# Kernel optimization log

Measured on AMD Instinct MI355X. Metric: run time of the kernel, lower is better.

Reference implementation:

```python
import jax, jax.numpy as jnp
import numpy as np

B, S = 64, 512
DC, DB = 200, 200            # embed_char_dim, embed_bichar_dim
HID = 300                    # linear out / lstm input
H = 300                      # rnn_hidden_dim
VC, VB = 10000, 200000       # char / bichar vocab
INPUT_DIM = (DC + DB) * 2    # 800


def lstm_scan(x_seq, W_hh):
    # x_seq: [S, B, 4H] = x @ W_ih.T + b_ih + b_hh, precomputed for all steps
    Bq = x_seq.shape[1]
    h0 = jnp.zeros((Bq, H), x_seq.dtype)
    c0 = jnp.zeros((Bq, H), x_seq.dtype)

    def step(carry, x_t):
        h, c = carry
        gates = x_t + h @ W_hh.T                 # [B, 4H]
        i, f, g, o = jnp.split(gates, 4, axis=-1)
        i = jax.nn.sigmoid(i)
        f = jax.nn.sigmoid(f)
        g = jnp.tanh(g)
        o = jax.nn.sigmoid(o)
        c = f * c + i * g
        h = o * jnp.tanh(c)
        return (h, c), h

    _, hs = jax.lax.scan(step, (h0, c0), x_seq)
    return hs                                    # [S, B, H]


def setup_inputs() -> dict:
    key = jax.random.key(0)
    ks = jax.random.split(key, 20)
    inp = {
        'char_features': jax.random.randint(ks[0], (B, S), 0, VC),
        'bichar_left_features': jax.random.randint(ks[1], (B, S), 0, VB),
        'bichar_right_features': jax.random.randint(ks[2], (B, S), 0, VB),
        'static_char_features': jax.random.randint(ks[3], (B, S), 0, VC),
        'static_bichar_left_features': jax.random.randint(ks[4], (B, S), 0, VB),
        'static_bichar_right_features': jax.random.randint(ks[5], (B, S), 0, VB),
        # embedding tables (padding-id row zeroing omitted; random rows)
        'char_embed': jax.random.normal(ks[6], (VC, DC), jnp.float32) * 0.1,
        'bichar_embed': jax.random.normal(ks[7], (VB, DB), jnp.float32) * 0.1,
        'static_char_embed': jax.random.uniform(ks[8], (VC, DC), jnp.float32, -0.12, 0.12),
        'static_bichar_embed': jax.random.uniform(ks[9], (VB, DB), jnp.float32, -0.12, 0.12),
        # linear: [HID, INPUT_DIM]
        'W_lin': jax.random.normal(ks[10], (HID, INPUT_DIM), jnp.float32) * (1.0 / np.sqrt(INPUT_DIM)),
        'b_lin': jax.random.normal(ks[11], (HID,), jnp.float32) * 0.01,
        # LSTM cells (b = b_ih + b_hh folded)
        'Wih_l': jax.random.normal(ks[12], (4 * H, HID), jnp.float32) * (1.0 / np.sqrt(HID)),
        'Whh_l': jax.random.normal(ks[13], (4 * H, H), jnp.float32) * (1.0 / np.sqrt(H)),
        'b_l': jax.random.normal(ks[14], (4 * H,), jnp.float32) * 0.01,
        'Wih_r': jax.random.normal(ks[15], (4 * H, HID), jnp.float32) * (1.0 / np.sqrt(HID)),
        'Whh_r': jax.random.normal(ks[16], (4 * H, H), jnp.float32) * (1.0 / np.sqrt(H)),
        'b_r': jax.random.normal(ks[17], (4 * H,), jnp.float32) * 0.01,
    }
    return inp


def reference(char_features, bichar_left_features, bichar_right_features,
              static_char_features, static_bichar_left_features, static_bichar_right_features,
              char_embed, bichar_embed, static_char_embed, static_bichar_embed,
              W_lin, b_lin, Wih_l, Whh_l, b_l, Wih_r, Whh_r, b_r):
    # embedding lookups (dropout is identity in eval mode)
    cf = char_embed[char_features]                       # [B,S,DC]
    scf = static_char_embed[static_char_features]        # [B,S,DC]
    bl = bichar_embed[bichar_left_features]              # [B,S,DB]
    br = bichar_embed[bichar_right_features]             # [B,S,DB]
    sbl = static_bichar_embed[static_bichar_left_features]
    sbr = static_bichar_embed[static_bichar_right_features]

    left = jnp.concatenate([cf, scf, bl, sbl], axis=-1)   # [B,S,INPUT_DIM]
    right = jnp.concatenate([cf, scf, br, sbr], axis=-1)
    left = jnp.tanh(left @ W_lin.T + b_lin)               # [B,S,HID]
    right = jnp.tanh(right @ W_lin.T + b_lin)

    # precompute input contributions for all timesteps, then scan the recurrence
    xl = jnp.einsum('bsd,gd->sbg', left, Wih_l) + b_l     # [S,B,4H]
    hs_l = lstm_scan(xl, Whh_l)                            # [S,B,H]

    xr = jnp.einsum('bsd,gd->sbg', right, Wih_r) + b_r
    hs_r = lstm_scan(xr[::-1], Whh_r)[::-1]               # right-to-left LSTM

    out = jnp.concatenate([hs_l.transpose(1, 0, 2), hs_r.transpose(1, 0, 2)], axis=-1)
    return out                                             # [B,S,2H]
```

## Files before the change

kernel.cpp:

```cpp
#include <hip/hip_runtime.h>
#include <hip/hip_bf16.h>

#define S_LEN 512
#define BATCH 64
#define DC    200
#define HID   300
#define H4    1200
#define IN_DIM 800
#define G_SPLIT 10

typedef __attribute__((ext_vector_type(8))) short short8b;
typedef __attribute__((ext_vector_type(4))) float f32x4;
typedef __attribute__((ext_vector_type(4))) int   i32x4;

__device__ __forceinline__ float sigmoidf_(float x) { return 1.0f / (1.0f + __expf(-x)); }
__device__ __forceinline__ float tanhf_(float x)    { return 2.0f / (1.0f + __expf(-2.0f * x)) - 1.0f; }

__global__ void k_prep_w(const float* __restrict__ Whh_l, const float* __restrict__ Whh_r,
                         const float* __restrict__ Wih_l, const float* __restrict__ Wih_r,
                         __hip_bfloat16* __restrict__ Whh_p, __hip_bfloat16* __restrict__ Wih_p) {
    int i = blockIdx.x * 256 + threadIdx.x;
    if (i >= 2 * 1280 * 320) return;
    int slot = i % 320;
    int R = (i / 320) % 1280;
    int d = i / (320 * 1280);
    int g = R >> 7, local = R & 127;
    float vh = 0.f, vi = 0.f;
    if (local < 120) {
        int q = local / 30, jj = local % 30;
        int n = q * 300 + g * 30 + jj;
        const float* Whh = d ? Whh_r : Whh_l;
        const float* Wih = d ? Wih_r : Wih_l;
        int g2 = slot >> 5, jj2 = slot & 31;
        if (jj2 < 30) vh = Whh[n * 300 + g2 * 30 + jj2];
        if (slot < 300) vi = Wih[n * 300 + slot];
    }
    Whh_p[i] = __float2bfloat16(vh);
    Wih_p[i] = __float2bfloat16(vi);
}

__global__ void k_prep_misc(const float* __restrict__ b_l, const float* __restrict__ b_r,
                            int* __restrict__ hb_st,
                            float* __restrict__ bias_p) {
    int i = blockIdx.x * 256 + threadIdx.x;
    if (i < 102400) hb_st[i] = 0;
    if (i < 2 * 1280) {
        int d = i / 1280, R = i % 1280;
        int g = R >> 7, local = R & 127;
        float v = 0.f;
        if (local < 120) { int q = local / 30, jj = local % 30; v = (d ? b_r : b_l)[q * 300 + g * 30 + jj]; }
        bias_p[i] = v;
    }
}

__global__ __launch_bounds__(256) void k_lin(
    const int* __restrict__ cf, const int* __restrict__ bl, const int* __restrict__ br,
    const int* __restrict__ scf, const int* __restrict__ sbl, const int* __restrict__ sbr,
    const float* __restrict__ ce, const float* __restrict__ be,
    const float* __restrict__ sce, const float* __restrict__ sbe,
    const float* __restrict__ W, const float* __restrict__ bias,
    __hip_bfloat16* __restrict__ outL, __hip_bfloat16* __restrict__ outR)
{
    const int z = blockIdx.y;
    const int* dynIdx  = z ? br  : bl;
    const int* statIdx = z ? sbr : sbl;
    __hip_bfloat16* outp = z ? outR : outL;
    const int m0 = blockIdx.x * 64;

    __shared__ __align__(16) __hip_bfloat16 sA[64][40];
    __shared__ __align__(16) __hip_bfloat16 sB[320][40];
    const int t = threadIdx.x, lane = t & 63, wv = t >> 6;

    const int rA = t >> 2, c8A = (t & 3) * 8;
    const int mA = m0 + rA;
    const int idc = cf[mA], idsc = scf[mA], idd = dynIdx[mA], ids = statIdx[mA];

    f32x4 acc[4][5] = {};

    for (int k0 = 0; k0 < IN_DIM; k0 += 32) {
        {
            int k = k0 + c8A;
            int seg = k / 200, kin = k - seg * 200;
            const float* tab = (seg == 0) ? ce : (seg == 1) ? sce : (seg == 2) ? be : sbe;
            int id = (seg == 0) ? idc : (seg == 1) ? idsc : (seg == 2) ? idd : ids;
            const float* tp = tab + (size_t)id * DC + kin;
            f32x4 v0 = *reinterpret_cast<const f32x4*>(tp);
            f32x4 v1 = *reinterpret_cast<const f32x4*>(tp + 4);
            union { short8b v; __hip_bfloat16 h[8]; } u;
#pragma unroll
            for (int q = 0; q < 4; ++q) { u.h[q] = __float2bfloat16(v0[q]); u.h[4 + q] = __float2bfloat16(v1[q]); }
            *reinterpret_cast<short8b*>(&sA[rA][c8A]) = u.v;
        }
#pragma unroll
        for (int j = 0; j < 5; ++j) {
            int i = t + j * 256;
            int n = i >> 2, ch = (i & 3) * 8;
            f32x4 v0 = {0, 0, 0, 0}, v1 = {0, 0, 0, 0};
            if (n < HID) {
                const float* wp = W + (size_t)n * IN_DIM + k0 + ch;
                v0 = *reinterpret_cast<const f32x4*>(wp);
                v1 = *reinterpret_cast<const f32x4*>(wp + 4);
            }
            union { short8b v; __hip_bfloat16 h[8]; } u;
#pragma unroll
            for (int q = 0; q < 4; ++q) { u.h[q] = __float2bfloat16(v0[q]); u.h[4 + q] = __float2bfloat16(v1[q]); }
            *reinterpret_cast<short8b*>(&sB[n][ch]) = u.v;
        }
        __syncthreads();
        const int kl = (lane >> 4) * 8, bb = lane & 15;
#pragma unroll
        for (int mt = 0; mt < 4; ++mt) {
            short8b af = *reinterpret_cast<const short8b*>(&sA[mt * 16 + bb][kl]);
#pragma unroll
            for (int nt = 0; nt < 5; ++nt) {
                short8b bf = *reinterpret_cast<const short8b*>(&sB[(wv * 5 + nt) * 16 + bb][kl]);
                acc[mt][nt] = __builtin_amdgcn_mfma_f32_16x16x32_bf16(af, bf, acc[mt][nt], 0, 0, 0);
            }
        }
        __syncthreads();
    }
    const int bb = lane & 15;
#pragma unroll
    for (int mt = 0; mt < 4; ++mt)
#pragma unroll
        for (int nt = 0; nt < 5; ++nt) {
            int p = (wv * 5 + nt) * 16 + bb;
            float bv = (p < HID) ? bias[p] : 0.f;
#pragma unroll
            for (int r = 0; r < 4; ++r) {
                int m = m0 + mt * 16 + (lane >> 4) * 4 + r;
                float val = (p < HID) ? tanhf_(acc[mt][nt][r] + bv) : 0.f;
                outp[(size_t)m * 320 + p] = __float2bfloat16(val);
            }
        }
}

__global__ __launch_bounds__(256) void k_xgemm(
    const __hip_bfloat16* __restrict__ A,
    const __hip_bfloat16* __restrict__ Wih_p,
    const float* __restrict__ bias_p,
    __hip_bfloat16* __restrict__ Xout)
{
    const int dir = blockIdx.z;
    const int m0 = blockIdx.x * 64;
    const int n0 = blockIdx.y * 128;
    const __hip_bfloat16* Ad = A + (size_t)dir * 32768 * 320;
    const __hip_bfloat16* Wd = Wih_p + (size_t)dir * 1280 * 320;
    const float* bd = bias_p + dir * 1280;
    __hip_bfloat16* Xd = Xout + (size_t)dir * 512 * 64 * 1280;

    __shared__ __align__(16) __hip_bfloat16 sA[64][40];
    __shared__ __align__(16) __hip_bfloat16 sB[128][40];
    const int t = threadIdx.x, lane = t & 63, wv = t >> 6;
    f32x4 acc[4][2] = {};

    for (int k0 = 0; k0 < 320; k0 += 32) {
        {
            int r = t >> 2, kg = (t & 3) * 8;
            *reinterpret_cast<short8b*>(&sA[r][kg]) =
                *reinterpret_cast<const short8b*>(Ad + (size_t)(m0 + r) * 320 + k0 + kg);
        }
#pragma unroll
        for (int i = 0; i < 2; ++i) {
            int c = t + i * 256;
            int r = c >> 2, kg = (c & 3) * 8;
            *reinterpret_cast<short8b*>(&sB[r][kg]) =
                *reinterpret_cast<const short8b*>(Wd + (size_t)(n0 + r) * 320 + k0 + kg);
        }
        __syncthreads();
        const int kl = (lane >> 4) * 8;
#pragma unroll
        for (int mt = 0; mt < 4; ++mt) {
            short8b af = *reinterpret_cast<const short8b*>(&sA[mt * 16 + (lane & 15)][kl]);
#pragma unroll
            for (int nt = 0; nt < 2; ++nt) {
                short8b bf = *reinterpret_cast<const short8b*>(&sB[(wv * 2 + nt) * 16 + (lane & 15)][kl]);
                acc[mt][nt] = __builtin_amdgcn_mfma_f32_16x16x32_bf16(af, bf, acc[mt][nt], 0, 0, 0);
            }
        }
        __syncthreads();
    }
#pragma unroll
    for (int mt = 0; mt < 4; ++mt)
#pragma unroll
        for (int nt = 0; nt < 2; ++nt) {
            int p = n0 + (wv * 2 + nt) * 16 + (lane & 15);
            float bv = bd[p];
#pragma unroll
            for (int r = 0; r < 4; ++r) {
                int m = m0 + mt * 16 + (lane >> 4) * 4 + r;
                int b = m >> 9, s = m & 511;
                Xd[(size_t)(s * 64 + b) * 1280 + p] = __float2bfloat16(acc[mt][nt][r] + bv);
            }
        }
}

__global__ __launch_bounds__(256) void k_rec(
    const __hip_bfloat16* __restrict__ X,
    const __hip_bfloat16* __restrict__ Whh_p,
    i32x4* __restrict__ hb_st,
    float* __restrict__ out)
{
    const int bid = blockIdx.x;
    const int dir = bid / (4 * G_SPLIT);
    const int grp = (bid / G_SPLIT) % 4;
    const int g   = bid % G_SPLIT;
    const int t = threadIdx.x;
    const int lane = t & 63, wv = t >> 6;
    const int b0 = grp * 16;

    __shared__ __align__(16) __hip_bfloat16 sHi[16][328];
    __shared__ __align__(16) __hip_bfloat16 sLo[16][328];
    __shared__ float sG[16][132];
    unsigned* sHiW = (unsigned*)sHi;
    unsigned* sLoW = (unsigned*)sLo;

    const int n0 = wv * 32;
    const int bb = lane & 15;
    const int hi4 = lane >> 4;

    short8b wB0[10], wB1[10];
    {
        const __hip_bfloat16* Wsrc = Whh_p + ((size_t)dir * 1280 + g * 128) * 320;
#pragma unroll
        for (int kt = 0; kt < 10; ++kt) {
            wB0[kt] = *reinterpret_cast<const short8b*>(Wsrc + (size_t)(n0 + bb) * 320 + kt * 32 + hi4 * 8);
            wB1[kt] = *reinterpret_cast<const short8b*>(Wsrc + (size_t)(n0 + 16 + bb) * 320 + kt * 32 + hi4 * 8);
        }
    }
    for (int i = t; i < 16 * 164; i += 256) { sHiW[i] = 0; sLoW[i] = 0; }
    __syncthreads();

    float cst[6] = {};

    __hip_bfloat16 xa[8];
    {
        const int s0 = dir ? (S_LEN - 1) : 0;
        const __hip_bfloat16* xp = X + (((size_t)dir * 512 + s0) * 64 + b0) * 1280 + g * 128;
#pragma unroll
        for (int r = 0; r < 4; ++r) {
            int m = hi4 * 4 + r;
            xa[r]     = xp[(size_t)m * 1280 + n0 + bb];
            xa[4 + r] = xp[(size_t)m * 1280 + n0 + 16 + bb];
        }
    }

    for (int tau = 0; tau < S_LEN; ++tau) {
        const int s = dir ? (S_LEN - 1 - tau) : tau;
        const int par = tau & 1;

        i32x4 ch[7];
        const i32x4* hbase = hb_st + ((size_t)(dir * 2 + par) * 64 + b0) * 100;
        for (;;) {
            bool ok = true;
#pragma unroll
            for (int k = 0; k < 7; ++k) {
                int idx = t + k * 256;
                if (idx < 1600)
                    asm volatile("global_load_dwordx4 %0, %1, off sc0 sc1"
                                 : "=v"(ch[k]) : "v"(hbase + idx) : "memory");
            }
            asm volatile("s_waitcnt vmcnt(0)" ::: "memory");
#pragma unroll
            for (int k = 0; k < 7; ++k) {
                int idx = t + k * 256;
                if (idx < 1600 && ch[k][0] != tau) ok = false;
            }
            if (ok) break;
            __builtin_amdgcn_s_sleep(1);
        }
        __builtin_amdgcn_sched_barrier(0);

#pragma unroll
        for (int k = 0; k < 7; ++k) {
            int idx = t + k * 256;
            if (idx < 1600) {
                int b = idx / 100, rem = idx - b * 100;
                int g2 = rem / 10, c = rem - g2 * 10;
                int chi = (c < 5) ? c : c - 5;
                unsigned* dst = ((c < 5) ? sHiW : sLoW) + b * 164 + g2 * 16 + chi * 3;
                dst[0] = (unsigned)ch[k][1];
                dst[1] = (unsigned)ch[k][2];
                dst[2] = (unsigned)ch[k][3];
            }
        }
        __syncthreads();

        f32x4 acc0, acc1;
#pragma unroll
        for (int r = 0; r < 4; ++r) {
            acc0[r] = __bfloat162float(xa[r]);
            acc1[r] = __bfloat162float(xa[4 + r]);
        }
#pragma unroll
        for (int kt = 0; kt < 10; ++kt) {
            short8b ahi = *reinterpret_cast<const short8b*>(&sHi[bb][kt * 32 + hi4 * 8]);
            short8b alo = *reinterpret_cast<const short8b*>(&sLo[bb][kt * 32 + hi4 * 8]);
            acc0 = __builtin_amdgcn_mfma_f32_16x16x32_bf16(ahi, wB0[kt], acc0, 0, 0, 0);
            acc1 = __builtin_amdgcn_mfma_f32_16x16x32_bf16(ahi, wB1[kt], acc1, 0, 0, 0);
            acc0 = __builtin_amdgcn_mfma_f32_16x16x32_bf16(alo, wB0[kt], acc0, 0, 0, 0);
            acc1 = __builtin_amdgcn_mfma_f32_16x16x32_bf16(alo, wB1[kt], acc1, 0, 0, 0);
        }
#pragma unroll
        for (int r = 0; r < 4; ++r) {
            int m = hi4 * 4 + r;
            sG[m][n0 + bb] = acc0[r];
            sG[m][n0 + 16 + bb] = acc1[r];
        }
        __syncthreads();

        if (t < 80) {
            int b = t / 5, c5 = t - (b * 5), jj0 = c5 * 6;
            float hv[6];
            unsigned hius[6], lous[6];
#pragma unroll
            for (int u = 0; u < 6; ++u) {
                int jj = jj0 + u;
                float ig = sigmoidf_(sG[b][jj]);
                float fg = sigmoidf_(sG[b][30 + jj]);
                float gg = tanhf_(sG[b][60 + jj]);
                float og = sigmoidf_(sG[b][90 + jj]);
                float cn = fg * cst[u] + ig * gg;
                cst[u] = cn;
                float h = og * tanhf_(cn);
                hv[u] = h;
                __hip_bfloat16 hb_ = __float2bfloat16(h);
                float lof = h - __bfloat162float(hb_);
                __hip_bfloat16 lb_ = __float2bfloat16(lof);
                union { __hip_bfloat16 x; unsigned short u16; } ch1{hb_}, ch2{lb_};
                hius[u] = ch1.u16;
                lous[u] = ch2.u16;
            }
            i32x4 dhi, dlo;
            dhi[0] = tau + 1; dhi[1] = (int)(hius[0] | (hius[1] << 16));
            dhi[2] = (int)(hius[2] | (hius[3] << 16)); dhi[3] = (int)(hius[4] | (hius[5] << 16));
            dlo[0] = tau + 1; dlo[1] = (int)(lous[0] | (lous[1] << 16));
            dlo[2] = (int)(lous[2] | (lous[3] << 16)); dlo[3] = (int)(lous[4] | (lous[5] << 16));
            i32x4* pb = hb_st + ((size_t)(dir * 2 + (par ^ 1)) * 64 + b0 + b) * 100 + g * 10 + c5;
            asm volatile("s_waitcnt vmcnt(0)" ::: "memory");
            asm volatile("global_store_dwordx4 %0, %1, off sc0 sc1" :: "v"(pb), "v"(dhi) : "memory");
            asm volatile("global_store_dwordx4 %0, %1, off sc0 sc1" :: "v"(pb + 5), "v"(dlo) : "memory");
            float* op = out + ((size_t)(b0 + b) * S_LEN + s) * 600 + dir * 300 + g * 30 + jj0;
#pragma unroll
            for (int u = 0; u < 6; ++u) op[u] = hv[u];
        }

        if (tau < S_LEN - 1) {
            const int sn = dir ? (s - 1) : (s + 1);
            const __hip_bfloat16* xp = X + (((size_t)dir * 512 + sn) * 64 + b0) * 1280 + g * 128;
#pragma unroll
            for (int r = 0; r < 4; ++r) {
                int m = hi4 * 4 + r;
                xa[r]     = xp[(size_t)m * 1280 + n0 + bb];
                xa[4 + r] = xp[(size_t)m * 1280 + n0 + 16 + bb];
            }
        }
    }
}

extern "C" void kernel_launch(void* const* d_in, const int* in_sizes, int n_in,
                              void* d_out, int out_size, void* d_ws, size_t ws_size,
                              hipStream_t stream) {
    const int*   cf    = (const int*)d_in[0];
    const int*   bl    = (const int*)d_in[1];
    const int*   br    = (const int*)d_in[2];
    const int*   scf   = (const int*)d_in[3];
    const int*   sbl   = (const int*)d_in[4];
    const int*   sbr   = (const int*)d_in[5];
    const float* ce    = (const float*)d_in[6];
    const float* be    = (const float*)d_in[7];
    const float* sce   = (const float*)d_in[8];
    const float* sbe   = (const float*)d_in[9];
    const float* Wlin  = (const float*)d_in[10];
    const float* blin  = (const float*)d_in[11];
    const float* Wih_l = (const float*)d_in[12];
    const float* Whh_l = (const float*)d_in[13];
    const float* b_l   = (const float*)d_in[14];
    const float* Wih_r = (const float*)d_in[15];
    const float* Whh_r = (const float*)d_in[16];
    const float* b_r   = (const float*)d_in[17];
    float* out = (float*)d_out;

    char* ws = (char*)d_ws;
    __hip_bfloat16* A_b    = (__hip_bfloat16*)(ws);
    __hip_bfloat16* A_l    = A_b;
    __hip_bfloat16* A_r    = A_b + (size_t)32768 * 320;
    __hip_bfloat16* X      = (__hip_bfloat16*)(ws + 41943040);
    __hip_bfloat16* Whh_p  = (__hip_bfloat16*)(ws + 209715200);
    __hip_bfloat16* Wih_p  = (__hip_bfloat16*)(ws + 211353600);
    float*          bias_p = (float*)(ws + 212992000);
    i32x4*          hb_st  = (i32x4*)(ws + 213002240);

    k_prep_w<<<dim3((2 * 1280 * 320 + 255) / 256), dim3(256), 0, stream>>>(
        Whh_l, Whh_r, Wih_l, Wih_r, Whh_p, Wih_p);
    k_prep_misc<<<dim3(1280), dim3(256), 0, stream>>>(b_l, b_r, (int*)hb_st, bias_p);
    k_lin<<<dim3(512, 2), dim3(256), 0, stream>>>(cf, bl, br, scf, sbl, sbr,
                                                  ce, be, sce, sbe, Wlin, blin,
                                                  A_l, A_r);
    k_xgemm<<<dim3(512, 10, 2), dim3(256), 0, stream>>>(A_b, Wih_p, bias_p, X);
    k_rec<<<dim3(80), dim3(256), 0, stream>>>(X, Whh_p, hb_st, out);
}
```

Before: 2.288 ms.

## Exchange hidden state via 8-byte atomics with packed step stamp

The cross-block hidden-state exchange in the recurrent kernel is rebuilt. Each 16-byte record that carried 6 values plus a separate stamp becomes an 8-byte record of 3 bf16 values with the stamp packed in the top half. Stores now use atomic swap and polling uses atomic OR with zero, and polling only retries chunks not yet seen. The gate-update stage is also split across 160 threads instead of 80. The aim is lower store-to-load visibility latency and less redundant polling traffic per step. The cost is roughly twice as many, smaller atomic operations per step, and the stamp is limited to 16 bits.

Result: slower. 2.981 ms (+30.3%).

```diff
diff --git a/kernel.cpp b/kernel.cpp
--- a/kernel.cpp
+++ b/kernel.cpp
@@ -11,7 +11,7 @@
 
 typedef __attribute__((ext_vector_type(8))) short short8b;
 typedef __attribute__((ext_vector_type(4))) float f32x4;
-typedef __attribute__((ext_vector_type(4))) int   i32x4;
+typedef __attribute__((ext_vector_type(2))) int   i32x2;
 
 __device__ __forceinline__ float sigmoidf_(float x) { return 1.0f / (1.0f + __expf(-x)); }
 __device__ __forceinline__ float tanhf_(float x)    { return 2.0f / (1.0f + __expf(-2.0f * x)) - 1.0f; }
@@ -40,10 +40,10 @@
 }
 
 __global__ void k_prep_misc(const float* __restrict__ b_l, const float* __restrict__ b_r,
-                            int* __restrict__ hb_st,
+                            int* __restrict__ hb,
                             float* __restrict__ bias_p) {
     int i = blockIdx.x * 256 + threadIdx.x;
-    if (i < 102400) hb_st[i] = 0;
+    if (i < 102400) hb[i] = 0;
     if (i < 2 * 1280) {
         int d = i / 1280, R = i % 1280;
         int g = R >> 7, local = R & 127;
@@ -198,7 +198,7 @@
 __global__ __launch_bounds__(256) void k_rec(
     const __hip_bfloat16* __restrict__ X,
     const __hip_bfloat16* __restrict__ Whh_p,
-    i32x4* __restrict__ hb_st,
+    i32x2* __restrict__ hb,
     float* __restrict__ out)
 {
     const int bid = blockIdx.x;
@@ -212,6 +212,8 @@
     __shared__ __align__(16) __hip_bfloat16 sHi[16][328];
     __shared__ __align__(16) __hip_bfloat16 sLo[16][328];
     __shared__ float sG[16][132];
+    unsigned short* sHiU = (unsigned short*)sHi;
+    unsigned short* sLoU = (unsigned short*)sLo;
     unsigned* sHiW = (unsigned*)sHi;
     unsigned* sLoW = (unsigned*)sLo;
 
@@ -231,7 +233,7 @@
     for (int i = t; i < 16 * 164; i += 256) { sHiW[i] = 0; sLoW[i] = 0; }
     __syncthreads();
 
-    float cst[6] = {};
+    float cst[3] = {};
 
     __hip_bfloat16 xa[8];
     {
@@ -245,43 +247,50 @@
         }
     }
 
+    const i32x2 zero2 = {0, 0};
+
     for (int tau = 0; tau < S_LEN; ++tau) {
         const int s = dir ? (S_LEN - 1 - tau) : tau;
         const int par = tau & 1;
 
-        i32x4 ch[7];
-        const i32x4* hbase = hb_st + ((size_t)(dir * 2 + par) * 64 + b0) * 100;
+        i32x2 q[13];
+        unsigned done = 0;
+        const i32x2* hbase = hb + ((size_t)(dir * 2 + par) * 64 + b0) * 200;
         for (;;) {
-            bool ok = true;
-#pragma unroll
-            for (int k = 0; k < 7; ++k) {
+#pragma unroll
+            for (int k = 0; k < 13; ++k) {
                 int idx = t + k * 256;
-                if (idx < 1600)
-                    asm volatile("global_load_dwordx4 %0, %1, off sc0 sc1"
-                                 : "=v"(ch[k]) : "v"(hbase + idx) : "memory");
+                if (idx < 3200 && !((done >> k) & 1))
+                    asm volatile("global_atomic_or_x2 %0, %1, %2, off sc0 sc1"
+                                 : "=v"(q[k]) : "v"(hbase + idx), "v"(zero2) : "memory");
             }
             asm volatile("s_waitcnt vmcnt(0)" ::: "memory");
-#pragma unroll
-            for (int k = 0; k < 7; ++k) {
+            bool all = true;
+#pragma unroll
+            for (int k = 0; k < 13; ++k) {
                 int idx = t + k * 256;
-                if (idx < 1600 && ch[k][0] != tau) ok = false;
-            }
-            if (ok) break;
+                if (idx < 3200 && !((done >> k) & 1)) {
+                    if ((((unsigned)q[k][1]) >> 16) == (unsigned)tau) done |= 1u << k;
+                    else all = false;
+                }
+            }
+            if (all) break;
             __builtin_amdgcn_s_sleep(1);
         }
         __builtin_amdgcn_sched_barrier(0);
 
 #pragma unroll
-        for (int k = 0; k < 7; ++k) {
+        for (int k = 0; k < 13; ++k) {
             int idx = t + k * 256;
-            if (idx < 1600) {
-                int b = idx / 100, rem = idx - b * 100;
-                int g2 = rem / 10, c = rem - g2 * 10;
-                int chi = (c < 5) ? c : c - 5;
-                unsigned* dst = ((c < 5) ? sHiW : sLoW) + b * 164 + g2 * 16 + chi * 3;
-                dst[0] = (unsigned)ch[k][1];
-                dst[1] = (unsigned)ch[k][2];
-                dst[2] = (unsigned)ch[k][3];
+            if (idx < 3200) {
+                int b = idx / 200, r = idx - b * 200;
+                int buf = r / 100, j = r - buf * 100;
+                int jt = j / 10;
+                int slot = jt * 32 + (j - jt * 10) * 3;
+                unsigned short* dst = (buf ? sLoU : sHiU) + b * 328 + slot;
+                dst[0] = (unsigned short)(q[k][0] & 0xffff);
+                dst[1] = (unsigned short)(((unsigned)q[k][0]) >> 16);
+                dst[2] = (unsigned short)(q[k][1] & 0xffff);
             }
         }
         __syncthreads();
@@ -309,13 +318,13 @@
         }
         __syncthreads();
 
-        if (t < 80) {
-            int b = t / 5, c5 = t - (b * 5), jj0 = c5 * 6;
-            float hv[6];
-            unsigned hius[6], lous[6];
-#pragma unroll
-            for (int u = 0; u < 6; ++u) {
-                int jj = jj0 + u;
+        if (t < 160) {
+            int b = t / 10, jq = t - b * 10;
+            float hv3[3];
+            unsigned hu[3], lu[3];
+#pragma unroll
+            for (int u = 0; u < 3; ++u) {
+                int jj = 3 * jq + u;
                 float ig = sigmoidf_(sG[b][jj]);
                 float fg = sigmoidf_(sG[b][30 + jj]);
                 float gg = tanhf_(sG[b][60 + jj]);
@@ -323,26 +332,25 @@
                 float cn = fg * cst[u] + ig * gg;
                 cst[u] = cn;
                 float h = og * tanhf_(cn);
-                hv[u] = h;
+                hv3[u] = h;
                 __hip_bfloat16 hb_ = __float2bfloat16(h);
                 float lof = h - __bfloat162float(hb_);
                 __hip_bfloat16 lb_ = __float2bfloat16(lof);
-                union { __hip_bfloat16 x; unsigned short u16; } ch1{hb_}, ch2{lb_};
-                hius[u] = ch1.u16;
-                lous[u] = ch2.u16;
-            }
-            i32x4 dhi, dlo;
-            dhi[0] = tau + 1; dhi[1] = (int)(hius[0] | (hius[1] << 16));
-            dhi[2] = (int)(hius[2] | (hius[3] << 16)); dhi[3] = (int)(hius[4] | (hius[5] << 16));
-            dlo[0] = tau + 1; dlo[1] = (int)(lous[0] | (lous[1] << 16));
-            dlo[2] = (int)(lous[2] | (lous[3] << 16)); dlo[3] = (int)(lous[4] | (lous[5] << 16));
-            i32x4* pb = hb_st + ((size_t)(dir * 2 + (par ^ 1)) * 64 + b0 + b) * 100 + g * 10 + c5;
-            asm volatile("s_waitcnt vmcnt(0)" ::: "memory");
-            asm volatile("global_store_dwordx4 %0, %1, off sc0 sc1" :: "v"(pb), "v"(dhi) : "memory");
-            asm volatile("global_store_dwordx4 %0, %1, off sc0 sc1" :: "v"(pb + 5), "v"(dlo) : "memory");
-            float* op = out + ((size_t)(b0 + b) * S_LEN + s) * 600 + dir * 300 + g * 30 + jj0;
-#pragma unroll
-            for (int u = 0; u < 6; ++u) op[u] = hv[u];
+                union { __hip_bfloat16 x; unsigned short u16; } c1{hb_}, c2{lb_};
+                hu[u] = c1.u16;
+                lu[u] = c2.u16;
+            }
+            unsigned stamp = (unsigned)(tau + 1);
+            i32x2 dhi, dlo;
+            dhi[0] = (int)(hu[0] | (hu[1] << 16));
+            dhi[1] = (int)(hu[2] | (stamp << 16));
+            dlo[0] = (int)(lu[0] | (lu[1] << 16));
+            dlo[1] = (int)(lu[2] | (stamp << 16));
+            i32x2* pb = hb + ((size_t)(dir * 2 + (par ^ 1)) * 64 + b0 + b) * 200 + g * 10 + jq;
+            asm volatile("global_atomic_swap_x2 %0, %1, off sc1" :: "v"(pb), "v"(dhi) : "memory");
+            asm volatile("global_atomic_swap_x2 %0, %1, off sc1" :: "v"(pb + 100), "v"(dlo) : "memory");
+            float* op = out + ((size_t)(b0 + b) * S_LEN + s) * 600 + dir * 300 + g * 30 + 3 * jq;
+            op[0] = hv3[0]; op[1] = hv3[1]; op[2] = hv3[2];
         }
 
         if (tau < S_LEN - 1) {
@@ -389,14 +397,14 @@
     __hip_bfloat16* Whh_p  = (__hip_bfloat16*)(ws + 209715200);
     __hip_bfloat16* Wih_p  = (__hip_bfloat16*)(ws + 211353600);
     float*          bias_p = (float*)(ws + 212992000);
-    i32x4*          hb_st  = (i32x4*)(ws + 213002240);
+    i32x2*          hb     = (i32x2*)(ws + 213002240);
 
     k_prep_w<<<dim3((2 * 1280 * 320 + 255) / 256), dim3(256), 0, stream>>>(
         Whh_l, Whh_r, Wih_l, Wih_r, Whh_p, Wih_p);
-    k_prep_misc<<<dim3(1280), dim3(256), 0, stream>>>(b_l, b_r, (int*)hb_st, bias_p);
+    k_prep_misc<<<dim3(1280), dim3(256), 0, stream>>>(b_l, b_r, (int*)hb, bias_p);
     k_lin<<<dim3(512, 2), dim3(256), 0, stream>>>(cf, bl, br, scf, sbl, sbr,
                                                   ce, be, sce, sbe, Wlin, blin,
                                                   A_l, A_r);
     k_xgemm<<<dim3(512, 10, 2), dim3(256), 0, stream>>>(A_b, Wih_p, bias_p, X);
-    k_rec<<<dim3(80), dim3(256), 0, stream>>>(X, Whh_p, hb_st, out);
-}
+    k_rec<<<dim3(80), dim3(256), 0, stream>>>(X, Whh_p, hb, out);
+}
```

## Store recurrent state chunks with flags in place and poll only missing chunks

Applied to the files above, without the earlier changes.

The recurrent hidden-state exchange now copies each 16-byte chunk, including its step flag, directly into shared memory. The W_hh matrix is repacked to a padded K of 416, with zero weights at the flag positions, so the MFMA loop runs 13 K-tiles instead of 10. This drops the unpack and scatter arithmetic per step. The spin-wait also stops reloading chunks that have already arrived. The cost is about 30% more MFMA work per step on the serial critical path and more weight registers.

After: 2.495 ms. +9.0%, slower.

```diff
diff --git a/kernel.cpp b/kernel.cpp
--- a/kernel.cpp
+++ b/kernel.cpp
@@ -8,6 +8,8 @@
 #define H4    1200
 #define IN_DIM 800
 #define G_SPLIT 10
+#define KP    416
+#define LPITCH 440
 
 typedef __attribute__((ext_vector_type(8))) short short8b;
 typedef __attribute__((ext_vector_type(4))) float f32x4;
@@ -20,30 +22,43 @@
                          const float* __restrict__ Wih_l, const float* __restrict__ Wih_r,
                          __hip_bfloat16* __restrict__ Whh_p, __hip_bfloat16* __restrict__ Wih_p) {
     int i = blockIdx.x * 256 + threadIdx.x;
-    if (i >= 2 * 1280 * 320) return;
-    int slot = i % 320;
-    int R = (i / 320) % 1280;
-    int d = i / (320 * 1280);
-    int g = R >> 7, local = R & 127;
-    float vh = 0.f, vi = 0.f;
-    if (local < 120) {
-        int q = local / 30, jj = local % 30;
-        int n = q * 300 + g * 30 + jj;
-        const float* Whh = d ? Whh_r : Whh_l;
-        const float* Wih = d ? Wih_r : Wih_l;
-        int g2 = slot >> 5, jj2 = slot & 31;
-        if (jj2 < 30) vh = Whh[n * 300 + g2 * 30 + jj2];
-        if (slot < 300) vi = Wih[n * 300 + slot];
-    }
-    Whh_p[i] = __float2bfloat16(vh);
-    Wih_p[i] = __float2bfloat16(vi);
+    if (i < 2 * 1280 * KP) {
+        int slot = i % KP;
+        int R = (i / KP) % 1280;
+        int d = i / (KP * 1280);
+        int g = R >> 7, local = R & 127;
+        float vh = 0.f;
+        int w = slot & 7;
+        if (local < 120 && slot < 400 && w >= 2) {
+            int c = slot >> 3;
+            int g2 = c / 5, cc = c - g2 * 5;
+            int dim = g2 * 30 + cc * 6 + (w - 2);
+            int q = local / 30, jj = local % 30;
+            int n = q * 300 + g * 30 + jj;
+            vh = (d ? Whh_r : Whh_l)[n * 300 + dim];
+        }
+        Whh_p[i] = __float2bfloat16(vh);
+    }
+    if (i < 2 * 1280 * 320) {
+        int slot = i % 320;
+        int R = (i / 320) % 1280;
+        int d = i / (320 * 1280);
+        int g = R >> 7, local = R & 127;
+        float vi = 0.f;
+        if (local < 120 && slot < 300) {
+            int q = local / 30, jj = local % 30;
+            int n = q * 300 + g * 30 + jj;
+            vi = (d ? Wih_r : Wih_l)[n * 300 + slot];
+        }
+        Wih_p[i] = __float2bfloat16(vi);
+    }
 }
 
 __global__ void k_prep_misc(const float* __restrict__ b_l, const float* __restrict__ b_r,
-                            int* __restrict__ hb_st,
+                            int* __restrict__ hb,
                             float* __restrict__ bias_p) {
     int i = blockIdx.x * 256 + threadIdx.x;
-    if (i < 102400) hb_st[i] = 0;
+    if (i < 102400) hb[i] = 0;
     if (i < 2 * 1280) {
         int d = i / 1280, R = i % 1280;
         int g = R >> 7, local = R & 127;
@@ -198,7 +213,7 @@
 __global__ __launch_bounds__(256) void k_rec(
     const __hip_bfloat16* __restrict__ X,
     const __hip_bfloat16* __restrict__ Whh_p,
-    i32x4* __restrict__ hb_st,
+    i32x4* __restrict__ hb,
     float* __restrict__ out)
 {
     const int bid = blockIdx.x;
@@ -209,26 +224,28 @@
     const int lane = t & 63, wv = t >> 6;
     const int b0 = grp * 16;
 
-    __shared__ __align__(16) __hip_bfloat16 sHi[16][328];
-    __shared__ __align__(16) __hip_bfloat16 sLo[16][328];
+    __shared__ __align__(16) short sHiS[16][LPITCH];
+    __shared__ __align__(16) short sLoS[16][LPITCH];
     __shared__ float sG[16][132];
-    unsigned* sHiW = (unsigned*)sHi;
-    unsigned* sLoW = (unsigned*)sLo;
 
     const int n0 = wv * 32;
     const int bb = lane & 15;
     const int hi4 = lane >> 4;
 
-    short8b wB0[10], wB1[10];
+    short8b wB0[13], wB1[13];
     {
-        const __hip_bfloat16* Wsrc = Whh_p + ((size_t)dir * 1280 + g * 128) * 320;
-#pragma unroll
-        for (int kt = 0; kt < 10; ++kt) {
-            wB0[kt] = *reinterpret_cast<const short8b*>(Wsrc + (size_t)(n0 + bb) * 320 + kt * 32 + hi4 * 8);
-            wB1[kt] = *reinterpret_cast<const short8b*>(Wsrc + (size_t)(n0 + 16 + bb) * 320 + kt * 32 + hi4 * 8);
-        }
-    }
-    for (int i = t; i < 16 * 164; i += 256) { sHiW[i] = 0; sLoW[i] = 0; }
+        const __hip_bfloat16* Wsrc = Whh_p + ((size_t)dir * 1280 + g * 128) * KP;
+#pragma unroll
+        for (int kt = 0; kt < 13; ++kt) {
+            wB0[kt] = *reinterpret_cast<const short8b*>(Wsrc + (size_t)(n0 + bb) * KP + kt * 32 + hi4 * 8);
+            wB1[kt] = *reinterpret_cast<const short8b*>(Wsrc + (size_t)(n0 + 16 + bb) * KP + kt * 32 + hi4 * 8);
+        }
+    }
+    {
+        int* zHi = (int*)sHiS;
+        int* zLo = (int*)sLoS;
+        for (int i = t; i < 16 * (LPITCH / 2); i += 256) { zHi[i] = 0; zLo[i] = 0; }
+    }
     __syncthreads();
 
     float cst[6] = {};
@@ -249,24 +266,28 @@
         const int s = dir ? (S_LEN - 1 - tau) : tau;
         const int par = tau & 1;
 
-        i32x4 ch[7];
-        const i32x4* hbase = hb_st + ((size_t)(dir * 2 + par) * 64 + b0) * 100;
+        i32x4 q[7];
+        unsigned done = 0;
+        const i32x4* hbase = hb + ((size_t)(dir * 2 + par) * 64 + b0) * 100;
         for (;;) {
-            bool ok = true;
 #pragma unroll
             for (int k = 0; k < 7; ++k) {
                 int idx = t + k * 256;
-                if (idx < 1600)
+                if (idx < 1600 && !((done >> k) & 1))
                     asm volatile("global_load_dwordx4 %0, %1, off sc0 sc1"
-                                 : "=v"(ch[k]) : "v"(hbase + idx) : "memory");
+                                 : "=v"(q[k]) : "v"(hbase + idx) : "memory");
             }
             asm volatile("s_waitcnt vmcnt(0)" ::: "memory");
+            bool all = true;
 #pragma unroll
             for (int k = 0; k < 7; ++k) {
                 int idx = t + k * 256;
-                if (idx < 1600 && ch[k][0] != tau) ok = false;
-            }
-            if (ok) break;
+                if (idx < 1600 && !((done >> k) & 1)) {
+                    if (q[k][0] == tau) done |= 1u << k;
+                    else all = false;
+                }
+            }
+            if (all) break;
             __builtin_amdgcn_s_sleep(1);
         }
         __builtin_amdgcn_sched_barrier(0);
@@ -275,13 +296,10 @@
         for (int k = 0; k < 7; ++k) {
             int idx = t + k * 256;
             if (idx < 1600) {
-                int b = idx / 100, rem = idx - b * 100;
-                int g2 = rem / 10, c = rem - g2 * 10;
-                int chi = (c < 5) ? c : c - 5;
-                unsigned* dst = ((c < 5) ? sHiW : sLoW) + b * 164 + g2 * 16 + chi * 3;
-                dst[0] = (unsigned)ch[k][1];
-                dst[1] = (unsigned)ch[k][2];
-                dst[2] = (unsigned)ch[k][3];
+                int b = idx / 100, r = idx - b * 100;
+                int c = (r < 50) ? r : r - 50;
+                short* dst = ((r < 50) ? &sHiS[b][0] : &sLoS[b][0]) + c * 8;
+                *reinterpret_cast<i32x4*>(dst) = q[k];
             }
         }
         __syncthreads();
@@ -293,9 +311,9 @@
             acc1[r] = __bfloat162float(xa[4 + r]);
         }
 #pragma unroll
-        for (int kt = 0; kt < 10; ++kt) {
-            short8b ahi = *reinterpret_cast<const short8b*>(&sHi[bb][kt * 32 + hi4 * 8]);
-            short8b alo = *reinterpret_cast<const short8b*>(&sLo[bb][kt * 32 + hi4 * 8]);
+        for (int kt = 0; kt < 13; ++kt) {
+            short8b ahi = *reinterpret_cast<const short8b*>(&sHiS[bb][kt * 32 + hi4 * 8]);
+            short8b alo = *reinterpret_cast<const short8b*>(&sLoS[bb][kt * 32 + hi4 * 8]);
             acc0 = __builtin_amdgcn_mfma_f32_16x16x32_bf16(ahi, wB0[kt], acc0, 0, 0, 0);
             acc1 = __builtin_amdgcn_mfma_f32_16x16x32_bf16(ahi, wB1[kt], acc1, 0, 0, 0);
             acc0 = __builtin_amdgcn_mfma_f32_16x16x32_bf16(alo, wB0[kt], acc0, 0, 0, 0);
@@ -310,7 +328,7 @@
         __syncthreads();
 
         if (t < 80) {
-            int b = t / 5, c5 = t - (b * 5), jj0 = c5 * 6;
+            int b = t / 5, cc = t - (b * 5), jj0 = cc * 6;
             float hv[6];
             unsigned hius[6], lous[6];
 #pragma unroll
@@ -336,10 +354,10 @@
             dhi[2] = (int)(hius[2] | (hius[3] << 16)); dhi[3] = (int)(hius[4] | (hius[5] << 16));
             dlo[0] = tau + 1; dlo[1] = (int)(lous[0] | (lous[1] << 16));
             dlo[2] = (int)(lous[2] | (lous[3] << 16)); dlo[3] = (int)(lous[4] | (lous[5] << 16));
-            i32x4* pb = hb_st + ((size_t)(dir * 2 + (par ^ 1)) * 64 + b0 + b) * 100 + g * 10 + c5;
+            i32x4* pb = hb + ((size_t)(dir * 2 + (par ^ 1)) * 64 + b0 + b) * 100 + g * 5 + cc;
             asm volatile("s_waitcnt vmcnt(0)" ::: "memory");
             asm volatile("global_store_dwordx4 %0, %1, off sc0 sc1" :: "v"(pb), "v"(dhi) : "memory");
-            asm volatile("global_store_dwordx4 %0, %1, off sc0 sc1" :: "v"(pb + 5), "v"(dlo) : "memory");
+            asm volatile("global_store_dwordx4 %0, %1, off sc0 sc1" :: "v"(pb + 50), "v"(dlo) : "memory");
             float* op = out + ((size_t)(b0 + b) * S_LEN + s) * 600 + dir * 300 + g * 30 + jj0;
 #pragma unroll
             for (int u = 0; u < 6; ++u) op[u] = hv[u];
@@ -387,16 +405,16 @@
     __hip_bfloat16* A_r    = A_b + (size_t)32768 * 320;
     __hip_bfloat16* X      = (__hip_bfloat16*)(ws + 41943040);
     __hip_bfloat16* Whh_p  = (__hip_bfloat16*)(ws + 209715200);
-    __hip_bfloat16* Wih_p  = (__hip_bfloat16*)(ws + 211353600);
-    float*          bias_p = (float*)(ws + 212992000);
-    i32x4*          hb_st  = (i32x4*)(ws + 213002240);
-
-    k_prep_w<<<dim3((2 * 1280 * 320 + 255) / 256), dim3(256), 0, stream>>>(
+    __hip_bfloat16* Wih_p  = (__hip_bfloat16*)(ws + 211845120);
+    float*          bias_p = (float*)(ws + 213483520);
+    i32x4*          hb     = (i32x4*)(ws + 213493760);
+
+    k_prep_w<<<dim3((2 * 1280 * KP + 255) / 256), dim3(256), 0, stream>>>(
         Whh_l, Whh_r, Wih_l, Wih_r, Whh_p, Wih_p);
-    k_prep_misc<<<dim3(1280), dim3(256), 0, stream>>>(b_l, b_r, (int*)hb_st, bias_p);
+    k_prep_misc<<<dim3(1280), dim3(256), 0, stream>>>(b_l, b_r, (int*)hb, bias_p);
     k_lin<<<dim3(512, 2), dim3(256), 0, stream>>>(cf, bl, br, scf, sbl, sbr,
                                                   ce, be, sce, sbe, Wlin, blin,
                                                   A_l, A_r);
     k_xgemm<<<dim3(512, 10, 2), dim3(256), 0, stream>>>(A_b, Wih_p, bias_p, X);
-    k_rec<<<dim3(80), dim3(256), 0, stream>>>(X, Whh_p, hb_st, out);
-}
+    k_rec<<<dim3(80), dim3(256), 0, stream>>>(X, Whh_p, hb, out);
+}
```

## Interleave two batch groups per recurrence block to hide cross-block sync latency

Applied to the files above, without the earlier changes.

The recurrent kernel now runs 40 blocks instead of 80. Each block handles two 16-row batch groups in alternating phases, so the wait on peer blocks for one group's hidden state overlaps with computing the other group's step. The spin-wait also stops re-polling chunks that already carry the expected step tag. The cost is twice as much serial MFMA and gate work per block per timestep, and half as many blocks active.

Measured after the change: 3.529 ms. 1.54x slower.

```diff
diff --git a/kernel.cpp b/kernel.cpp
--- a/kernel.cpp
+++ b/kernel.cpp
@@ -40,10 +40,10 @@
 }
 
 __global__ void k_prep_misc(const float* __restrict__ b_l, const float* __restrict__ b_r,
-                            int* __restrict__ hb_st,
+                            int* __restrict__ hb,
                             float* __restrict__ bias_p) {
     int i = blockIdx.x * 256 + threadIdx.x;
-    if (i < 102400) hb_st[i] = 0;
+    if (i < 102400) hb[i] = 0;
     if (i < 2 * 1280) {
         int d = i / 1280, R = i % 1280;
         int g = R >> 7, local = R & 127;
@@ -195,19 +195,131 @@
         }
 }
 
+#define PHASE(B0, CST, XA)                                                          \
+  {                                                                                 \
+    const int par = tau & 1;                                                        \
+    const int s = dir ? (S_LEN - 1 - tau) : tau;                                    \
+    i32x4 q[7];                                                                     \
+    unsigned done = 0;                                                              \
+    const i32x4* hbase = hb + ((size_t)(dir * 2 + par) * 64 + (B0)) * 100;          \
+    for (;;) {                                                                      \
+      _Pragma("unroll")                                                             \
+      for (int k = 0; k < 7; ++k) {                                                 \
+        int idx = t + k * 256;                                                      \
+        if (idx < 1600 && !((done >> k) & 1))                                       \
+          asm volatile("global_load_dwordx4 %0, %1, off sc0 sc1"                    \
+                       : "=v"(q[k]) : "v"(hbase + idx) : "memory");                 \
+      }                                                                             \
+      asm volatile("s_waitcnt vmcnt(0)" ::: "memory");                              \
+      bool all = true;                                                              \
+      _Pragma("unroll")                                                             \
+      for (int k = 0; k < 7; ++k) {                                                 \
+        int idx = t + k * 256;                                                      \
+        if (idx < 1600 && !((done >> k) & 1)) {                                     \
+          if (q[k][0] == tau) done |= 1u << k; else all = false;                    \
+        }                                                                           \
+      }                                                                             \
+      if (all) break;                                                               \
+      __builtin_amdgcn_s_sleep(1);                                                  \
+    }                                                                               \
+    __builtin_amdgcn_sched_barrier(0);                                              \
+    _Pragma("unroll")                                                               \
+    for (int k = 0; k < 7; ++k) {                                                   \
+      int idx = t + k * 256;                                                        \
+      if (idx < 1600) {                                                             \
+        int b = idx / 100, rem = idx - b * 100;                                     \
+        int g2 = rem / 10, c = rem - g2 * 10;                                       \
+        int chi = (c < 5) ? c : c - 5;                                              \
+        unsigned* dst = ((c < 5) ? sHiW : sLoW) + b * 164 + g2 * 16 + chi * 3;      \
+        dst[0] = (unsigned)q[k][1];                                                 \
+        dst[1] = (unsigned)q[k][2];                                                 \
+        dst[2] = (unsigned)q[k][3];                                                 \
+      }                                                                             \
+    }                                                                               \
+    __syncthreads();                                                                \
+    f32x4 acc0, acc1;                                                               \
+    _Pragma("unroll")                                                               \
+    for (int r = 0; r < 4; ++r) {                                                   \
+      acc0[r] = __bfloat162float(XA[r]);                                            \
+      acc1[r] = __bfloat162float(XA[4 + r]);                                        \
+    }                                                                               \
+    _Pragma("unroll")                                                               \
+    for (int kt = 0; kt < 10; ++kt) {                                               \
+      short8b ahi = *reinterpret_cast<const short8b*>(&sHi[bb][kt * 32 + hi4 * 8]); \
+      short8b alo = *reinterpret_cast<const short8b*>(&sLo[bb][kt * 32 + hi4 * 8]); \
+      acc0 = __builtin_amdgcn_mfma_f32_16x16x32_bf16(ahi, wB0[kt], acc0, 0, 0, 0);  \
+      acc1 = __builtin_amdgcn_mfma_f32_16x16x32_bf16(ahi, wB1[kt], acc1, 0, 0, 0);  \
+      acc0 = __builtin_amdgcn_mfma_f32_16x16x32_bf16(alo, wB0[kt], acc0, 0, 0, 0);  \
+      acc1 = __builtin_amdgcn_mfma_f32_16x16x32_bf16(alo, wB1[kt], acc1, 0, 0, 0);  \
+    }                                                                               \
+    _Pragma("unroll")                                                               \
+    for (int r = 0; r < 4; ++r) {                                                   \
+      int m = hi4 * 4 + r;                                                          \
+      sG[m][n0 + bb] = acc0[r];                                                     \
+      sG[m][n0 + 16 + bb] = acc1[r];                                                \
+    }                                                                               \
+    __syncthreads();                                                                \
+    if (t < 80) {                                                                   \
+      int b = t / 5, c5 = t - (b * 5), jj0 = c5 * 6;                                \
+      float hv[6];                                                                  \
+      unsigned hius[6], lous[6];                                                    \
+      _Pragma("unroll")                                                             \
+      for (int u = 0; u < 6; ++u) {                                                 \
+        int jj = jj0 + u;                                                           \
+        float ig = sigmoidf_(sG[b][jj]);                                            \
+        float fg = sigmoidf_(sG[b][30 + jj]);                                       \
+        float gg = tanhf_(sG[b][60 + jj]);                                          \
+        float og = sigmoidf_(sG[b][90 + jj]);                                       \
+        float cn = fg * (CST)[u] + ig * gg;                                         \
+        (CST)[u] = cn;                                                              \
+        float h = og * tanhf_(cn);                                                  \
+        hv[u] = h;                                                                  \
+        __hip_bfloat16 hb_ = __float2bfloat16(h);                                   \
+        float lof = h - __bfloat162float(hb_);                                      \
+        __hip_bfloat16 lb_ = __float2bfloat16(lof);                                 \
+        union { __hip_bfloat16 x; unsigned short u16; } ch1{hb_}, ch2{lb_};         \
+        hius[u] = ch1.u16; lous[u] = ch2.u16;                                       \
+      }                                                                             \
+      i32x4 dhi, dlo;                                                               \
+      dhi[0] = tau + 1; dhi[1] = (int)(hius[0] | (hius[1] << 16));                  \
+      dhi[2] = (int)(hius[2] | (hius[3] << 16)); dhi[3] = (int)(hius[4] | (hius[5] << 16)); \
+      dlo[0] = tau + 1; dlo[1] = (int)(lous[0] | (lous[1] << 16));                  \
+      dlo[2] = (int)(lous[2] | (lous[3] << 16)); dlo[3] = (int)(lous[4] | (lous[5] << 16)); \
+      i32x4* pb = hb + ((size_t)(dir * 2 + (par ^ 1)) * 64 + (B0) + b) * 100 + g * 10 + c5; \
+      asm volatile("s_waitcnt vmcnt(0)" ::: "memory");                              \
+      asm volatile("global_store_dwordx4 %0, %1, off sc0 sc1" :: "v"(pb), "v"(dhi) : "memory");     \
+      asm volatile("global_store_dwordx4 %0, %1, off sc0 sc1" :: "v"(pb + 5), "v"(dlo) : "memory"); \
+      float* op = out + ((size_t)((B0) + b) * S_LEN + s) * 600 + dir * 300 + g * 30 + jj0;  \
+      _Pragma("unroll")                                                             \
+      for (int u = 0; u < 6; ++u) op[u] = hv[u];                                    \
+    }                                                                               \
+    if (tau < S_LEN - 1) {                                                          \
+      const int sn = dir ? (s - 1) : (s + 1);                                       \
+      const __hip_bfloat16* xp = X + (((size_t)dir * 512 + sn) * 64 + (B0)) * 1280 + g * 128; \
+      _Pragma("unroll")                                                             \
+      for (int r = 0; r < 4; ++r) {                                                 \
+        int m = hi4 * 4 + r;                                                        \
+        (XA)[r]     = xp[(size_t)m * 1280 + n0 + bb];                               \
+        (XA)[4 + r] = xp[(size_t)m * 1280 + n0 + 16 + bb];                          \
+      }                                                                             \
+    }                                                                               \
+  }
+
 __global__ __launch_bounds__(256) void k_rec(
     const __hip_bfloat16* __restrict__ X,
     const __hip_bfloat16* __restrict__ Whh_p,
-    i32x4* __restrict__ hb_st,
+    i32x4* __restrict__ hb,
     float* __restrict__ out)
 {
     const int bid = blockIdx.x;
-    const int dir = bid / (4 * G_SPLIT);
-    const int grp = (bid / G_SPLIT) % 4;
+    const int set = bid / G_SPLIT;
     const int g   = bid % G_SPLIT;
+    const int dir = set >> 1;
+    const int gp  = set & 1;
+    const int b0A = gp * 32;
+    const int b0B = gp * 32 + 16;
     const int t = threadIdx.x;
     const int lane = t & 63, wv = t >> 6;
-    const int b0 = grp * 16;
 
     __shared__ __align__(16) __hip_bfloat16 sHi[16][328];
     __shared__ __align__(16) __hip_bfloat16 sLo[16][328];
@@ -231,130 +343,26 @@
     for (int i = t; i < 16 * 164; i += 256) { sHiW[i] = 0; sLoW[i] = 0; }
     __syncthreads();
 
-    float cst[6] = {};
-
-    __hip_bfloat16 xa[8];
+    float cstA[6] = {}, cstB[6] = {};
+
+    __hip_bfloat16 xaA[8], xaB[8];
     {
         const int s0 = dir ? (S_LEN - 1) : 0;
-        const __hip_bfloat16* xp = X + (((size_t)dir * 512 + s0) * 64 + b0) * 1280 + g * 128;
+        const __hip_bfloat16* xpA = X + (((size_t)dir * 512 + s0) * 64 + b0A) * 1280 + g * 128;
+        const __hip_bfloat16* xpB = X + (((size_t)dir * 512 + s0) * 64 + b0B) * 1280 + g * 128;
 #pragma unroll
         for (int r = 0; r < 4; ++r) {
             int m = hi4 * 4 + r;
-            xa[r]     = xp[(size_t)m * 1280 + n0 + bb];
-            xa[4 + r] = xp[(size_t)m * 1280 + n0 + 16 + bb];
+            xaA[r]     = xpA[(size_t)m * 1280 + n0 + bb];
+            xaA[4 + r] = xpA[(size_t)m * 1280 + n0 + 16 + bb];
+            xaB[r]     = xpB[(size_t)m * 1280 + n0 + bb];
+            xaB[4 + r] = xpB[(size_t)m * 1280 + n0 + 16 + bb];
         }
     }
 
     for (int tau = 0; tau < S_LEN; ++tau) {
-        const int s = dir ? (S_LEN - 1 - tau) : tau;
-        const int par = tau & 1;
-
-        i32x4 ch[7];
-        const i32x4* hbase = hb_st + ((size_t)(dir * 2 + par) * 64 + b0) * 100;
-        for (;;) {
-            bool ok = true;
-#pragma unroll
-            for (int k = 0; k < 7; ++k) {
-                int idx = t + k * 256;
-                if (idx < 1600)
-                    asm volatile("global_load_dwordx4 %0, %1, off sc0 sc1"
-                                 : "=v"(ch[k]) : "v"(hbase + idx) : "memory");
-            }
-            asm volatile("s_waitcnt vmcnt(0)" ::: "memory");
-#pragma unroll
-            for (int k = 0; k < 7; ++k) {
-                int idx = t + k * 256;
-                if (idx < 1600 && ch[k][0] != tau) ok = false;
-            }
-            if (ok) break;
-            __builtin_amdgcn_s_sleep(1);
-        }
-        __builtin_amdgcn_sched_barrier(0);
-
-#pragma unroll
-        for (int k = 0; k < 7; ++k) {
-            int idx = t + k * 256;
-            if (idx < 1600) {
-                int b = idx / 100, rem = idx - b * 100;
-                int g2 = rem / 10, c = rem - g2 * 10;
-                int chi = (c < 5) ? c : c - 5;
-                unsigned* dst = ((c < 5) ? sHiW : sLoW) + b * 164 + g2 * 16 + chi * 3;
-                dst[0] = (unsigned)ch[k][1];
-                dst[1] = (unsigned)ch[k][2];
-                dst[2] = (unsigned)ch[k][3];
-            }
-        }
-        __syncthreads();
-
-        f32x4 acc0, acc1;
-#pragma unroll
-        for (int r = 0; r < 4; ++r) {
-            acc0[r] = __bfloat162float(xa[r]);
-            acc1[r] = __bfloat162float(xa[4 + r]);
-        }
-#pragma unroll
-        for (int kt = 0; kt < 10; ++kt) {
-            short8b ahi = *reinterpret_cast<const short8b*>(&sHi[bb][kt * 32 + hi4 * 8]);
-            short8b alo = *reinterpret_cast<const short8b*>(&sLo[bb][kt * 32 + hi4 * 8]);
-            acc0 = __builtin_amdgcn_mfma_f32_16x16x32_bf16(ahi, wB0[kt], acc0, 0, 0, 0);
-            acc1 = __builtin_amdgcn_mfma_f32_16x16x32_bf16(ahi, wB1[kt], acc1, 0, 0, 0);
-            acc0 = __builtin_amdgcn_mfma_f32_16x16x32_bf16(alo, wB0[kt], acc0, 0, 0, 0);
-            acc1 = __builtin_amdgcn_mfma_f32_16x16x32_bf16(alo, wB1[kt], acc1, 0, 0, 0);
-        }
-#pragma unroll
-        for (int r = 0; r < 4; ++r) {
-            int m = hi4 * 4 + r;
-            sG[m][n0 + bb] = acc0[r];
-            sG[m][n0 + 16 + bb] = acc1[r];
-        }
-        __syncthreads();
-
-        if (t < 80) {
-            int b = t / 5, c5 = t - (b * 5), jj0 = c5 * 6;
-            float hv[6];
-            unsigned hius[6], lous[6];
-#pragma unroll
-            for (int u = 0; u < 6; ++u) {
-                int jj = jj0 + u;
-                float ig = sigmoidf_(sG[b][jj]);
-                float fg = sigmoidf_(sG[b][30 + jj]);
-                float gg = tanhf_(sG[b][60 + jj]);
-                float og = sigmoidf_(sG[b][90 + jj]);
-                float cn = fg * cst[u] + ig * gg;
-                cst[u] = cn;
-                float h = og * tanhf_(cn);
-                hv[u] = h;
-                __hip_bfloat16 hb_ = __float2bfloat16(h);
-                float lof = h - __bfloat162float(hb_);
-                __hip_bfloat16 lb_ = __float2bfloat16(lof);
-                union { __hip_bfloat16 x; unsigned short u16; } ch1{hb_}, ch2{lb_};
-                hius[u] = ch1.u16;
-                lous[u] = ch2.u16;
-            }
-            i32x4 dhi, dlo;
-            dhi[0] = tau + 1; dhi[1] = (int)(hius[0] | (hius[1] << 16));
-            dhi[2] = (int)(hius[2] | (hius[3] << 16)); dhi[3] = (int)(hius[4] | (hius[5] << 16));
-            dlo[0] = tau + 1; dlo[1] = (int)(lous[0] | (lous[1] << 16));
-            dlo[2] = (int)(lous[2] | (lous[3] << 16)); dlo[3] = (int)(lous[4] | (lous[5] << 16));
-            i32x4* pb = hb_st + ((size_t)(dir * 2 + (par ^ 1)) * 64 + b0 + b) * 100 + g * 10 + c5;
-            asm volatile("s_waitcnt vmcnt(0)" ::: "memory");
-            asm volatile("global_store_dwordx4 %0, %1, off sc0 sc1" :: "v"(pb), "v"(dhi) : "memory");
-            asm volatile("global_store_dwordx4 %0, %1, off sc0 sc1" :: "v"(pb + 5), "v"(dlo) : "memory");
-            float* op = out + ((size_t)(b0 + b) * S_LEN + s) * 600 + dir * 300 + g * 30 + jj0;
-#pragma unroll
-            for (int u = 0; u < 6; ++u) op[u] = hv[u];
-        }
-
-        if (tau < S_LEN - 1) {
-            const int sn = dir ? (s - 1) : (s + 1);
-            const __hip_bfloat16* xp = X + (((size_t)dir * 512 + sn) * 64 + b0) * 1280 + g * 128;
-#pragma unroll
-            for (int r = 0; r < 4; ++r) {
-                int m = hi4 * 4 + r;
-                xa[r]     = xp[(size_t)m * 1280 + n0 + bb];
-                xa[4 + r] = xp[(size_t)m * 1280 + n0 + 16 + bb];
-            }
-        }
+        PHASE(b0A, cstA, xaA);
+        PHASE(b0B, cstB, xaB);
     }
 }
 
@@ -389,14 +397,14 @@
     __hip_bfloat16* Whh_p  = (__hip_bfloat16*)(ws + 209715200);
     __hip_bfloat16* Wih_p  = (__hip_bfloat16*)(ws + 211353600);
     float*          bias_p = (float*)(ws + 212992000);
-    i32x4*          hb_st  = (i32x4*)(ws + 213002240);
+    i32x4*          hb     = (i32x4*)(ws + 213002240);
 
     k_prep_w<<<dim3((2 * 1280 * 320 + 255) / 256), dim3(256), 0, stream>>>(
         Whh_l, Whh_r, Wih_l, Wih_r, Whh_p, Wih_p);
-    k_prep_misc<<<dim3(1280), dim3(256), 0, stream>>>(b_l, b_r, (int*)hb_st, bias_p);
+    k_prep_misc<<<dim3(1280), dim3(256), 0, stream>>>(b_l, b_r, (int*)hb, bias_p);
     k_lin<<<dim3(512, 2), dim3(256), 0, stream>>>(cf, bl, br, scf, sbl, sbr,
                                                   ce, be, sce, sbe, Wlin, blin,
                                                   A_l, A_r);
     k_xgemm<<<dim3(512, 10, 2), dim3(256), 0, stream>>>(A_b, Wih_p, bias_p, X);
-    k_rec<<<dim3(80), dim3(256), 0, stream>>>(X, Whh_p, hb_st, out);
-}
+    k_rec<<<dim3(40), dim3(256), 0, stream>>>(X, Whh_p, hb, out);
+}
```
